# Optimization experiments

Hardware: AMD Instinct MI355X
Metric: run time of the kernel (lower is better)

The kernel has to match this reference:

```python
import jax, jax.numpy as jnp
import numpy as np

N_NODES = 50000

def _gcn_layer(x, src, dst, W, b, n_nodes):
    # x: [N, F_in]; src/dst: [E+N] (self-loops already appended)
    h = x @ W  # [N, F_out]
    deg = jax.ops.segment_sum(jnp.ones_like(dst, dtype=h.dtype), dst, num_segments=n_nodes)
    dinv = jnp.where(deg > 0, jax.lax.rsqrt(deg), 0.0)  # deg^{-1/2}
    norm = dinv[src] * dinv[dst]  # [E+N]
    msg = h[src] * norm[:, None]  # gather + scale
    out = jax.ops.segment_sum(msg, dst, num_segments=n_nodes)  # scatter-add
    return out + b

def setup_inputs() -> dict:
    key = jax.random.key(0)
    k1, k2, k3, k4 = jax.random.split(key, 4)
    d = 128
    E = 800000
    x = jax.random.normal(k1, (N_NODES, d), dtype=jnp.float32)
    edge_index = jax.random.randint(k2, (2, E), 0, N_NODES, dtype=jnp.int64)
    W1 = jax.random.normal(k3, (d, d), dtype=jnp.float32) / np.sqrt(d)
    b1 = jnp.zeros((d,), dtype=jnp.float32)
    W2 = jax.random.normal(k4, (d, d), dtype=jnp.float32) / np.sqrt(d)
    b2 = jnp.zeros((d,), dtype=jnp.float32)
    return {"x": x, "edge_index": edge_index, "W1": W1, "b1": b1, "W2": W2, "b2": b2}

def reference(x, edge_index, W1, b1, W2, b2):
    n = x.shape[0]
    loops = jnp.arange(n, dtype=edge_index.dtype)
    src = jnp.concatenate([edge_index[0], loops])  # add self-loops
    dst = jnp.concatenate([edge_index[1], loops])
    h = _gcn_layer(x, src, dst, W1, b1, n)
    h = jax.nn.relu(h)
    z = _gcn_layer(h, src, dst, W2, b2, n)
    return z
```

## Files before the change

kernel.cpp:

```cpp
#include <hip/hip_runtime.h>
#include <hip/hip_fp16.h>

#define NF 128
#define KC 64
#define NPART 4
#define NPMAX 12544

typedef _Float16 half8  __attribute__((ext_vector_type(8)));
typedef _Float16 half4v __attribute__((ext_vector_type(4)));
typedef float    floatx4 __attribute__((ext_vector_type(4)));

__global__ __launch_bounds__(512) void count2_k(
    const int* __restrict__ dst, unsigned char* __restrict__ pcnt,
    int E, int N, int Ec)
{
    __shared__ int lcnt[NPMAX];
    const int p = blockIdx.x & 3, c = blockIdx.x >> 2;
    const int Np = (N + 3) >> 2;
    const int lo = p * Np, hi = min(lo + Np, N);
    const int sz = hi - lo;
    for (int i = threadIdx.x; i < sz; i += 512) lcnt[i] = 0;
    __syncthreads();

    const int e0 = c * Ec, e1 = min(e0 + Ec, E);
    for (int e = e0 + (int)threadIdx.x * 4; e + 3 < e1; e += 512 * 4) {
        int4 d = *(const int4*)(dst + e);
        if (d.x >= lo && d.x < hi) atomicAdd(&lcnt[d.x - lo], 1);
        if (d.y >= lo && d.y < hi) atomicAdd(&lcnt[d.y - lo], 1);
        if (d.z >= lo && d.z < hi) atomicAdd(&lcnt[d.z - lo], 1);
        if (d.w >= lo && d.w < hi) atomicAdd(&lcnt[d.w - lo], 1);
    }
    int rem0 = e0 + ((e1 - e0) & ~3);
    for (int e = rem0 + (int)threadIdx.x; e < e1; e += 512) {
        int d = dst[e];
        if (d >= lo && d < hi) atomicAdd(&lcnt[d - lo], 1);
    }
    __syncthreads();
    for (int i = threadIdx.x; i < sz; i += 512)
        pcnt[(size_t)c * N + lo + i] = (unsigned char)lcnt[i];
}

__global__ __launch_bounds__(256) void pscan2_k(
    unsigned char* __restrict__ pcnt, float* __restrict__ dinv,
    int* __restrict__ rowptr, int* __restrict__ blocksum, int n, int N, int nb,
    const float* __restrict__ W1, const float* __restrict__ W2,
    __half* __restrict__ WT1, __half* __restrict__ WT2)
{
    if ((int)blockIdx.x >= nb) {
        int idx = ((int)blockIdx.x - nb) * 256 + threadIdx.x;
        const float* W = (idx < 16384) ? W1 : W2;
        __half* WT     = (idx < 16384) ? WT1 : WT2;
        int j = idx & 16383;
        int nn = j & 127, k = j >> 7;
        WT[nn * NF + k] = __float2half(W[k * NF + nn]);
        return;
    }
    __shared__ int sm[256];
    int tid = threadIdx.x;
    int bin = blockIdx.x * 256 + tid;
    int total = 0;
    if (bin < n) {
        #pragma unroll 4
        for (int c = 0; c < KC; c++) {
            size_t o = (size_t)c * N + bin;
            int v = pcnt[o];
            pcnt[o] = (unsigned char)total;
            total += v;
        }
        dinv[bin] = rsqrtf((float)total + 1.0f);
    }
    sm[tid] = total;
    __syncthreads();
    #pragma unroll
    for (int d = 1; d < 256; d <<= 1) {
        int t = (tid >= d) ? sm[tid - d] : 0;
        __syncthreads();
        sm[tid] += t;
        __syncthreads();
    }
    if (bin < n) rowptr[bin] = sm[tid] - total;
    if (tid == 255) blocksum[blockIdx.x] = sm[255];
}

template<bool F32IN>
__device__ __forceinline__ void gemm_body512(
    const void* __restrict__ Xv, const __half* __restrict__ WT,
    const float* __restrict__ dinv, __half* __restrict__ out, int M, int bid,
    __half (*wlds)[136])
{
    const int tid = threadIdx.x;
    {
        int r = tid >> 2;
        int c0 = (tid & 3) * 32;
        const half8* s = (const half8*)(WT + (size_t)r * NF + c0);
        half8* d = (half8*)&wlds[r][c0];
        #pragma unroll
        for (int j = 0; j < 4; j++) d[j] = s[j];
    }
    __syncthreads();

    const int wave = tid >> 6, lane = tid & 63;
    const int quad = lane >> 4, l15 = lane & 15;
    const int rowA = bid * 128 + wave * 16 + l15;
    const int rowc = (rowA < M) ? rowA : (M - 1);

    half8 afr[4];
    if (F32IN) {
        const float* X = (const float*)Xv;
        #pragma unroll
        for (int kc = 0; kc < 4; kc++) {
            const floatx4* p = (const floatx4*)(X + (size_t)rowc * NF + kc * 32 + quad * 8);
            floatx4 u = p[0], v = p[1];
            half8 a;
            a[0] = (_Float16)u[0]; a[1] = (_Float16)u[1];
            a[2] = (_Float16)u[2]; a[3] = (_Float16)u[3];
            a[4] = (_Float16)v[0]; a[5] = (_Float16)v[1];
            a[6] = (_Float16)v[2]; a[7] = (_Float16)v[3];
            afr[kc] = a;
        }
    } else {
        const __half* X = (const __half*)Xv;
        #pragma unroll
        for (int kc = 0; kc < 4; kc++)
            afr[kc] = *(const half8*)(X + (size_t)rowc * NF + kc * 32 + quad * 8);
    }

    floatx4 acc[8];
    #pragma unroll
    for (int ct = 0; ct < 8; ct++) { floatx4 z = {0.f, 0.f, 0.f, 0.f}; acc[ct] = z; }

    #pragma unroll
    for (int kc = 0; kc < 4; kc++) {
        #pragma unroll
        for (int ct = 0; ct < 8; ct++) {
            half8 b = *(const half8*)&wlds[ct * 16 + l15][kc * 32 + quad * 8];
            acc[ct] = __builtin_amdgcn_mfma_f32_16x16x32_f16(afr[kc], b, acc[ct], 0, 0, 0);
        }
    }

    const int orow0 = bid * 128 + wave * 16 + quad * 4;
    #pragma unroll
    for (int r = 0; r < 4; r++) {
        int orow = orow0 + r;
        if (orow < M) {
            float s = dinv[orow];
            #pragma unroll
            for (int ct = 0; ct < 8; ct++)
                out[(size_t)orow * NF + ct * 16 + l15] = __float2half(acc[ct][r] * s);
        }
    }
}

__global__ __launch_bounds__(512) void mid_k(
    const int* __restrict__ src, const int* __restrict__ dst,
    const int* __restrict__ rowptr, const unsigned char* __restrict__ coff,
    const int* __restrict__ blocksum, int* __restrict__ rowptr2,
    int* __restrict__ csr, int E, int N, int Ec, int nb,
    const float* __restrict__ X, const __half* __restrict__ WT,
    const float* __restrict__ dinv, __half* __restrict__ H, int GB2)
{
    __shared__ __align__(16) char smem[NPMAX * 4 + 1024];
    const int tid = threadIdx.x;
    if ((int)blockIdx.x < GB2) {
        gemm_body512<true>(X, WT, dinv, H, N, blockIdx.x, (__half(*)[136])smem);
        return;
    }
    int* lcur = (int*)smem;
    int* pref = (int*)(smem + NPMAX * 4);

    const int b = blockIdx.x - GB2;
    const int p = b & 3, c = b >> 2;
    const int Np = (N + 3) >> 2;
    const int lo = p * Np, hi = min(lo + Np, N);
    const int sz = hi - lo;

    int v = (tid < nb) ? blocksum[tid] : 0;
    if (tid < 256) pref[tid] = v;
    __syncthreads();
    #pragma unroll
    for (int d = 1; d < 256; d <<= 1) {
        int t = (tid < 256 && tid >= d) ? pref[tid - d] : 0;
        __syncthreads();
        if (tid < 256) pref[tid] += t;
        __syncthreads();
    }
    if (tid < 256) pref[tid] -= v;
    __syncthreads();

    for (int i = tid; i < sz; i += 512) {
        int bin = lo + i;
        int r = rowptr[bin] + pref[bin >> 8] + (int)coff[(size_t)c * N + bin];
        lcur[i] = r;
        if (c == 0) rowptr2[bin] = r;
    }
    if (c == 0 && p == 0 && tid == 0) rowptr2[N] = E;
    __syncthreads();

    const int e0 = c * Ec, e1 = min(e0 + Ec, E);
    for (int e = e0 + tid * 4; e + 3 < e1; e += 512 * 4) {
        int4 d = *(const int4*)(dst + e);
        int4 s = *(const int4*)(src + e);
        if (d.x >= lo && d.x < hi) csr[atomicAdd(&lcur[d.x - lo], 1)] = s.x;
        if (d.y >= lo && d.y < hi) csr[atomicAdd(&lcur[d.y - lo], 1)] = s.y;
        if (d.z >= lo && d.z < hi) csr[atomicAdd(&lcur[d.z - lo], 1)] = s.z;
        if (d.w >= lo && d.w < hi) csr[atomicAdd(&lcur[d.w - lo], 1)] = s.w;
    }
    int rem0 = e0 + ((e1 - e0) & ~3);
    for (int e = rem0 + tid; e < e1; e += 512) {
        int d = dst[e];
        if (d >= lo && d < hi) csr[atomicAdd(&lcur[d - lo], 1)] = src[e];
    }
}

__device__ __forceinline__ floatx4 gather_acc(
    const half4v* __restrict__ hs4, const int* __restrict__ csr,
    int base, int cnt, int node, int eg, int fl, int lane)
{
    floatx4 acc = {0.f, 0.f, 0.f, 0.f};
    int m0 = min(64, cnt);
    int idx0 = 0;
    if (lane < m0) idx0 = __builtin_nontemporal_load(&csr[base + lane]);
    if (eg == 0) {
        half4v s = hs4[(size_t)node * 32 + fl];
        acc[0] = (float)s[0]; acc[1] = (float)s[1];
        acc[2] = (float)s[2]; acc[3] = (float)s[3];
    }
    for (int off = 0; off < cnt; off += 64) {
        int m = min(64, cnt - off);
        int idx = (off == 0) ? idx0 : 0;
        if (off && lane < m) idx = __builtin_nontemporal_load(&csr[base + off + lane]);
        for (int j = 0; j < m; j += 16) {
            int s[8];
            half4v v[8];
            #pragma unroll
            for (int t = 0; t < 8; t++)
                s[t] = __shfl(idx, min(j + 2 * t + eg, m - 1), 64);
            #pragma unroll
            for (int t = 0; t < 8; t++)
                v[t] = hs4[(size_t)s[t] * 32 + fl];
            #pragma unroll
            for (int t = 0; t < 8; t++) {
                if (j + 2 * t + eg < m) {
                    acc[0] += (float)v[t][0]; acc[1] += (float)v[t][1];
                    acc[2] += (float)v[t][2]; acc[3] += (float)v[t][3];
                }
            }
        }
    }
    #pragma unroll
    for (int k = 0; k < 4; k++) acc[k] += __shfl_xor(acc[k], 32, 64);
    return acc;
}

__global__ __launch_bounds__(256) void agg_k(
    const __half* __restrict__ hs, const int* __restrict__ rowptr,
    const int* __restrict__ csr, const float* __restrict__ dinv,
    const float* __restrict__ bias, __half* __restrict__ outh,
    float* __restrict__ outf, int n)
{
    int wave = threadIdx.x >> 6;
    int lane = threadIdx.x & 63;
    int node = blockIdx.x * 4 + wave;
    if (node >= n) return;
    const int eg = lane >> 5, fl = lane & 31;

    int base = rowptr[node];
    int cnt  = rowptr[node + 1] - base;
    floatx4 acc = gather_acc((const half4v*)hs, csr, base, cnt, node, eg, fl, lane);

    if (eg == 0) {
        float dv = dinv[node];
        float o0 = dv * acc[0] + bias[fl * 4 + 0];
        float o1 = dv * acc[1] + bias[fl * 4 + 1];
        float o2 = dv * acc[2] + bias[fl * 4 + 2];
        float o3 = dv * acc[3] + bias[fl * 4 + 3];
        if (outh) {
            half4v h;
            h[0] = (_Float16)fmaxf(o0, 0.f); h[1] = (_Float16)fmaxf(o1, 0.f);
            h[2] = (_Float16)fmaxf(o2, 0.f); h[3] = (_Float16)fmaxf(o3, 0.f);
            *(half4v*)&outh[(size_t)node * NF + fl * 4] = h;
        } else {
            floatx4 w = {o0, o1, o2, o3};
            *(floatx4*)(outf + (size_t)node * NF + fl * 4) = w;
        }
    }
}

__global__ __launch_bounds__(256) void aggmm_k(
    const __half* __restrict__ hs, const int* __restrict__ rowptr,
    const int* __restrict__ csr, const float* __restrict__ dinv,
    const float* __restrict__ bias, const __half* __restrict__ WT,
    __half* __restrict__ Hout, int n)
{
    __shared__ __half alds[16][136];
    const int tid = threadIdx.x;
    const int wave = tid >> 6, lane = tid & 63;
    const int eg = lane >> 5, fl = lane & 31;
    const int nb0 = blockIdx.x * 16;

    #pragma unroll 1
    for (int q = 0; q < 4; q++) {
        int node = nb0 + wave * 4 + q;
        if (node < n) {
            int base = rowptr[node];
            int cnt  = rowptr[node + 1] - base;
            floatx4 acc = gather_acc((const half4v*)hs, csr, base, cnt, node, eg, fl, lane);
            if (eg == 0) {
                float dv = dinv[node];
                half4v h;
                h[0] = (_Float16)fmaxf(dv * acc[0] + bias[fl * 4 + 0], 0.f);
                h[1] = (_Float16)fmaxf(dv * acc[1] + bias[fl * 4 + 1], 0.f);
                h[2] = (_Float16)fmaxf(dv * acc[2] + bias[fl * 4 + 2], 0.f);
                h[3] = (_Float16)fmaxf(dv * acc[3] + bias[fl * 4 + 3], 0.f);
                *(half4v*)&alds[wave * 4 + q][fl * 4] = h;
            }
        } else if (eg == 0) {
            half4v z = {(_Float16)0.f, (_Float16)0.f, (_Float16)0.f, (_Float16)0.f};
            *(half4v*)&alds[wave * 4 + q][fl * 4] = z;
        }
    }
    __syncthreads();

    const int quad = lane >> 4, l15 = lane & 15;
    half8 afr[4];
    #pragma unroll
    for (int kc = 0; kc < 4; kc++)
        afr[kc] = *(const half8*)&alds[l15][kc * 32 + quad * 8];

    floatx4 acc0 = {0.f, 0.f, 0.f, 0.f};
    floatx4 acc1 = {0.f, 0.f, 0.f, 0.f};
    const int ct0 = wave * 2, ct1 = wave * 2 + 1;
    #pragma unroll
    for (int kc = 0; kc < 4; kc++) {
        half8 b0 = *(const half8*)(WT + (size_t)(ct0 * 16 + l15) * NF + kc * 32 + quad * 8);
        half8 b1 = *(const half8*)(WT + (size_t)(ct1 * 16 + l15) * NF + kc * 32 + quad * 8);
        acc0 = __builtin_amdgcn_mfma_f32_16x16x32_f16(afr[kc], b0, acc0, 0, 0, 0);
        acc1 = __builtin_amdgcn_mfma_f32_16x16x32_f16(afr[kc], b1, acc1, 0, 0, 0);
    }

    #pragma unroll
    for (int r = 0; r < 4; r++) {
        int row = quad * 4 + r;
        int node = nb0 + row;
        if (node < n) {
            float s = dinv[node];
            Hout[(size_t)node * NF + ct0 * 16 + l15] = __float2half(acc0[r] * s);
            Hout[(size_t)node * NF + ct1 * 16 + l15] = __float2half(acc1[r] * s);
        }
    }
}


extern "C" void kernel_launch(void* const* d_in, const int* in_sizes, int n_in,
                              void* d_out, int out_size, void* d_ws, size_t ws_size,
                              hipStream_t stream) {
    const float* x  = (const float*)d_in[0];
    const int*   ei = (const int*)d_in[1];
    const float* W1 = (const float*)d_in[2];
    const float* b1 = (const float*)d_in[3];
    const float* W2 = (const float*)d_in[4];
    const float* b2 = (const float*)d_in[5];
    float* out = (float*)d_out;

    const int N = in_sizes[0] / NF;
    const int E = in_sizes[1] / 2;
    const int* src = ei;
    const int* dst = ei + E;

    char* ws = (char*)d_ws;
    size_t off = 0;
    auto alloc = [&](size_t bytes) {
        void* p = ws + off;
        off += bytes;
        off = (off + 63) & ~(size_t)63;
        return p;
    };
    unsigned char* pcnt = (unsigned char*)alloc((size_t)KC * N);
    int*    rowptr  = (int*)alloc((size_t)(N + 1) * 4);
    int*    rowptr2 = (int*)alloc((size_t)(N + 1) * 4);
    int*    csr     = (int*)alloc((size_t)E * 4);
    float*  dinv    = (float*)alloc((size_t)N * 4);
    int*    bsum    = (int*)alloc((size_t)256 * 4);
    __half* WT1     = (__half*)alloc((size_t)NF * NF * 2);
    __half* WT2     = (__half*)alloc((size_t)NF * NF * 2);
    __half* H16     = (__half*)alloc((size_t)N * NF * 2);
    __half* A16     = (__half*)alloc((size_t)N * NF * 2);

    int nb  = (N + 255) / 256;
    int Ec  = (((E + KC - 1) / KC) + 3) & ~3;
    int GB2 = (N + 127) / 128;
    int fb  = (N + 15) / 16;
    int ab  = (N + 3) / 4;

    count2_k<<<KC * NPART, 512, 0, stream>>>(dst, pcnt, E, N, Ec);
    pscan2_k<<<nb + 128, 256, 0, stream>>>(pcnt, dinv, rowptr, bsum, N, N, nb,
                                           W1, W2, WT1, WT2);
    mid_k<<<GB2 + KC * NPART, 512, 0, stream>>>(src, dst, rowptr, pcnt, bsum,
                                                rowptr2, csr, E, N, Ec, nb,
                                                x, WT1, dinv, H16, GB2);
    aggmm_k<<<fb, 256, 0, stream>>>(H16, rowptr2, csr, dinv, b1, WT2, A16, N);
    agg_k<<<ab, 256, 0, stream>>>(A16, rowptr2, csr, dinv, b2, nullptr, out, N);
}
```

Measured before the change: 206.9 us.

## Sort CSR neighbor lists and interleave gathers across four nodes per wave

Adds a bitonic sort kernel that orders each node's source indices inside 64-entry chunks, so gathered rows come in ascending address order and may get better cache locality. The gather routine is replaced by one that processes four nodes per wave at once, interleaving their neighbor loads to raise memory-level parallelism. The final aggregation kernel now handles 16 nodes per block this way. This costs an extra kernel launch and a sort pass over the whole CSR. Small-degree nodes also lose the 8-wide unrolled batch of loads.

```diff
diff --git a/kernel.cpp b/kernel.cpp
--- a/kernel.cpp
+++ b/kernel.cpp
@@ -212,77 +212,103 @@
     }
 }
 
-__device__ __forceinline__ floatx4 gather_acc(
-    const half4v* __restrict__ hs4, const int* __restrict__ csr,
-    int base, int cnt, int node, int eg, int fl, int lane)
-{
-    floatx4 acc = {0.f, 0.f, 0.f, 0.f};
-    int m0 = min(64, cnt);
-    int idx0 = 0;
-    if (lane < m0) idx0 = __builtin_nontemporal_load(&csr[base + lane]);
-    if (eg == 0) {
-        half4v s = hs4[(size_t)node * 32 + fl];
-        acc[0] = (float)s[0]; acc[1] = (float)s[1];
-        acc[2] = (float)s[2]; acc[3] = (float)s[3];
-    }
+__global__ __launch_bounds__(256) void bsort_k(
+    const int* __restrict__ rowptr, int* __restrict__ csr, int n)
+{
+    int wave = threadIdx.x >> 6, lane = threadIdx.x & 63;
+    int node = blockIdx.x * 4 + wave;
+    if (node >= n) return;
+    int base = rowptr[node], cnt = rowptr[node + 1] - base;
     for (int off = 0; off < cnt; off += 64) {
         int m = min(64, cnt - off);
-        int idx = (off == 0) ? idx0 : 0;
-        if (off && lane < m) idx = __builtin_nontemporal_load(&csr[base + off + lane]);
-        for (int j = 0; j < m; j += 16) {
-            int s[8];
-            half4v v[8];
+        if (m <= 1) break;
+        int v = (lane < m) ? csr[base + off + lane] : 0x7fffffff;
+        #pragma unroll
+        for (int k = 2; k <= 64; k <<= 1) {
             #pragma unroll
-            for (int t = 0; t < 8; t++)
-                s[t] = __shfl(idx, min(j + 2 * t + eg, m - 1), 64);
-            #pragma unroll
-            for (int t = 0; t < 8; t++)
-                v[t] = hs4[(size_t)s[t] * 32 + fl];
-            #pragma unroll
-            for (int t = 0; t < 8; t++) {
-                if (j + 2 * t + eg < m) {
-                    acc[0] += (float)v[t][0]; acc[1] += (float)v[t][1];
-                    acc[2] += (float)v[t][2]; acc[3] += (float)v[t][3];
+            for (int j = k >> 1; j >= 1; j >>= 1) {
+                int pv = __shfl_xor(v, j, 64);
+                bool up = ((lane & k) == 0);
+                bool mn = (((lane & j) == 0) == up);
+                v = mn ? min(v, pv) : max(v, pv);
+            }
+        }
+        if (lane < m) csr[base + off + lane] = v;
+    }
+}
+
+__device__ __forceinline__ void gather4s(
+    const half4v* __restrict__ hs4, const int* __restrict__ csr,
+    const int* __restrict__ rowptr, int node0, int n,
+    int eg, int fl, int lane, floatx4 acc[4])
+{
+    int base[4], cc[4], rc[4], idx[4];
+    int maxc = 0;
+    #pragma unroll
+    for (int k = 0; k < 4; k++) {
+        int nd = node0 + k;
+        int b0 = 0, c0 = 0;
+        if (nd < n) { b0 = rowptr[nd]; c0 = rowptr[nd + 1] - b0; }
+        base[k] = b0; rc[k] = c0; cc[k] = min(c0, 64);
+        maxc = max(maxc, cc[k]);
+    }
+    #pragma unroll
+    for (int k = 0; k < 4; k++)
+        idx[k] = (lane < cc[k]) ? __builtin_nontemporal_load(&csr[base[k] + lane]) : 0;
+
+    #pragma unroll
+    for (int k = 0; k < 4; k++) { floatx4 z = {0.f, 0.f, 0.f, 0.f}; acc[k] = z; }
+
+    if (eg == 0) {
+        #pragma unroll
+        for (int k = 0; k < 4; k++) {
+            int nd = node0 + k;
+            if (nd < n) {
+                half4v s = hs4[(size_t)nd * 32 + fl];
+                acc[k][0] += (float)s[0]; acc[k][1] += (float)s[1];
+                acc[k][2] += (float)s[2]; acc[k][3] += (float)s[3];
+            }
+        }
+    }
+
+    const int rmax = (maxc + 1) >> 1;
+    #pragma unroll 2
+    for (int s = 0; s < rmax; s++) {
+        const int e2 = s * 2;
+        #pragma unroll
+        for (int k = 0; k < 4; k++) {
+            if (e2 < cc[k]) {
+                int si = __shfl(idx[k], min(e2 + eg, cc[k] - 1), 64);
+                half4v v = hs4[(size_t)si * 32 + fl];
+                if (e2 + eg < cc[k]) {
+                    acc[k][0] += (float)v[0]; acc[k][1] += (float)v[1];
+                    acc[k][2] += (float)v[2]; acc[k][3] += (float)v[3];
                 }
             }
         }
     }
-    #pragma unroll
-    for (int k = 0; k < 4; k++) acc[k] += __shfl_xor(acc[k], 32, 64);
-    return acc;
-}
-
-__global__ __launch_bounds__(256) void agg_k(
-    const __half* __restrict__ hs, const int* __restrict__ rowptr,
-    const int* __restrict__ csr, const float* __restrict__ dinv,
-    const float* __restrict__ bias, __half* __restrict__ outh,
-    float* __restrict__ outf, int n)
-{
-    int wave = threadIdx.x >> 6;
-    int lane = threadIdx.x & 63;
-    int node = blockIdx.x * 4 + wave;
-    if (node >= n) return;
-    const int eg = lane >> 5, fl = lane & 31;
-
-    int base = rowptr[node];
-    int cnt  = rowptr[node + 1] - base;
-    floatx4 acc = gather_acc((const half4v*)hs, csr, base, cnt, node, eg, fl, lane);
-
-    if (eg == 0) {
-        float dv = dinv[node];
-        float o0 = dv * acc[0] + bias[fl * 4 + 0];
-        float o1 = dv * acc[1] + bias[fl * 4 + 1];
-        float o2 = dv * acc[2] + bias[fl * 4 + 2];
-        float o3 = dv * acc[3] + bias[fl * 4 + 3];
-        if (outh) {
-            half4v h;
-            h[0] = (_Float16)fmaxf(o0, 0.f); h[1] = (_Float16)fmaxf(o1, 0.f);
-            h[2] = (_Float16)fmaxf(o2, 0.f); h[3] = (_Float16)fmaxf(o3, 0.f);
-            *(half4v*)&outh[(size_t)node * NF + fl * 4] = h;
-        } else {
-            floatx4 w = {o0, o1, o2, o3};
-            *(floatx4*)(outf + (size_t)node * NF + fl * 4) = w;
-        }
+
+    #pragma unroll
+    for (int k = 0; k < 4; k++) {
+        for (int off = 64; off < rc[k]; off += 64) {
+            int m = min(64, rc[k] - off);
+            int id2 = (lane < m) ? __builtin_nontemporal_load(&csr[base[k] + off + lane]) : 0;
+            for (int j = 0; j < m; j += 2) {
+                int si = __shfl(id2, min(j + eg, m - 1), 64);
+                half4v v = hs4[(size_t)si * 32 + fl];
+                if (j + eg < m) {
+                    acc[k][0] += (float)v[0]; acc[k][1] += (float)v[1];
+                    acc[k][2] += (float)v[2]; acc[k][3] += (float)v[3];
+                }
+            }
+        }
+    }
+
+    #pragma unroll
+    for (int k = 0; k < 4; k++) {
+        #pragma unroll
+        for (int q = 0; q < 4; q++)
+            acc[k][q] += __shfl_xor(acc[k][q], 32, 64);
     }
 }
 
@@ -297,26 +323,27 @@
     const int wave = tid >> 6, lane = tid & 63;
     const int eg = lane >> 5, fl = lane & 31;
     const int nb0 = blockIdx.x * 16;
-
-    #pragma unroll 1
-    for (int q = 0; q < 4; q++) {
-        int node = nb0 + wave * 4 + q;
-        if (node < n) {
-            int base = rowptr[node];
-            int cnt  = rowptr[node + 1] - base;
-            floatx4 acc = gather_acc((const half4v*)hs, csr, base, cnt, node, eg, fl, lane);
-            if (eg == 0) {
+    const int node0 = nb0 + wave * 4;
+
+    floatx4 acc[4];
+    gather4s((const half4v*)hs, csr, rowptr, node0, n, eg, fl, lane, acc);
+
+    if (eg == 0) {
+        #pragma unroll
+        for (int k = 0; k < 4; k++) {
+            int node = node0 + k;
+            half4v h;
+            if (node < n) {
                 float dv = dinv[node];
-                half4v h;
-                h[0] = (_Float16)fmaxf(dv * acc[0] + bias[fl * 4 + 0], 0.f);
-                h[1] = (_Float16)fmaxf(dv * acc[1] + bias[fl * 4 + 1], 0.f);
-                h[2] = (_Float16)fmaxf(dv * acc[2] + bias[fl * 4 + 2], 0.f);
-                h[3] = (_Float16)fmaxf(dv * acc[3] + bias[fl * 4 + 3], 0.f);
-                *(half4v*)&alds[wave * 4 + q][fl * 4] = h;
-            }
-        } else if (eg == 0) {
-            half4v z = {(_Float16)0.f, (_Float16)0.f, (_Float16)0.f, (_Float16)0.f};
-            *(half4v*)&alds[wave * 4 + q][fl * 4] = z;
+                h[0] = (_Float16)fmaxf(dv * acc[k][0] + bias[fl * 4 + 0], 0.f);
+                h[1] = (_Float16)fmaxf(dv * acc[k][1] + bias[fl * 4 + 1], 0.f);
+                h[2] = (_Float16)fmaxf(dv * acc[k][2] + bias[fl * 4 + 2], 0.f);
+                h[3] = (_Float16)fmaxf(dv * acc[k][3] + bias[fl * 4 + 3], 0.f);
+            } else {
+                h[0] = (_Float16)0.f; h[1] = (_Float16)0.f;
+                h[2] = (_Float16)0.f; h[3] = (_Float16)0.f;
+            }
+            *(half4v*)&alds[wave * 4 + k][fl * 4] = h;
         }
     }
     __syncthreads();
@@ -346,6 +373,36 @@
             float s = dinv[node];
             Hout[(size_t)node * NF + ct0 * 16 + l15] = __float2half(acc0[r] * s);
             Hout[(size_t)node * NF + ct1 * 16 + l15] = __float2half(acc1[r] * s);
+        }
+    }
+}
+
+__global__ __launch_bounds__(256) void agg4_k(
+    const __half* __restrict__ hs, const int* __restrict__ rowptr,
+    const int* __restrict__ csr, const float* __restrict__ dinv,
+    const float* __restrict__ bias, float* __restrict__ outf, int n)
+{
+    const int tid = threadIdx.x;
+    const int wave = tid >> 6, lane = tid & 63;
+    const int eg = lane >> 5, fl = lane & 31;
+    const int node0 = blockIdx.x * 16 + wave * 4;
+
+    floatx4 acc[4];
+    gather4s((const half4v*)hs, csr, rowptr, node0, n, eg, fl, lane, acc);
+
+    if (eg == 0) {
+        #pragma unroll
+        for (int k = 0; k < 4; k++) {
+            int node = node0 + k;
+            if (node < n) {
+                float dv = dinv[node];
+                floatx4 w;
+                w[0] = dv * acc[k][0] + bias[fl * 4 + 0];
+                w[1] = dv * acc[k][1] + bias[fl * 4 + 1];
+                w[2] = dv * acc[k][2] + bias[fl * 4 + 2];
+                w[3] = dv * acc[k][3] + bias[fl * 4 + 3];
+                *(floatx4*)(outf + (size_t)node * NF + fl * 4) = w;
+            }
         }
     }
 }
@@ -389,8 +446,8 @@
     int nb  = (N + 255) / 256;
     int Ec  = (((E + KC - 1) / KC) + 3) & ~3;
     int GB2 = (N + 127) / 128;
+    int sb  = (N + 3) / 4;
     int fb  = (N + 15) / 16;
-    int ab  = (N + 3) / 4;
 
     count2_k<<<KC * NPART, 512, 0, stream>>>(dst, pcnt, E, N, Ec);
     pscan2_k<<<nb + 128, 256, 0, stream>>>(pcnt, dinv, rowptr, bsum, N, N, nb,
@@ -398,6 +455,7 @@
     mid_k<<<GB2 + KC * NPART, 512, 0, stream>>>(src, dst, rowptr, pcnt, bsum,
                                                 rowptr2, csr, E, N, Ec, nb,
                                                 x, WT1, dinv, H16, GB2);
+    bsort_k<<<sb, 256, 0, stream>>>(rowptr2, csr, N);
     aggmm_k<<<fb, 256, 0, stream>>>(H16, rowptr2, csr, dinv, b1, WT2, A16, N);
-    agg_k<<<ab, 256, 0, stream>>>(A16, rowptr2, csr, dinv, b2, nullptr, out, N);
-}
+    agg4_k<<<fb, 256, 0, stream>>>(A16, rowptr2, csr, dinv, b2, out, N);
+}
```

Result: slower. 233.3 us (+12.8%).

## Gather eight nodes per wave with double-buffered interleaved loads in aggregation kernels

Applied to the files above, without the earlier changes.

Both aggregation kernels now give each wave eight destination nodes and keep two sets of eight gather loads in flight, alternating between them, so memory latency is hidden across nodes rather than within one node's short edge list. The aggmm kernel grows to 32 nodes per block with four MFMA tiles per wave, and the final layer uses a matching agg4 kernel. Nodes with more than 64 neighbours fall back to a serial tail loop. The cost is much higher register pressure, which is mitigated with a launch bound of four blocks per CU, and lanes idle when degrees within a group of eight differ.

```diff
diff --git a/kernel.cpp b/kernel.cpp
--- a/kernel.cpp
+++ b/kernel.cpp
@@ -212,141 +212,212 @@
     }
 }
 
-__device__ __forceinline__ floatx4 gather_acc(
-    const half4v* __restrict__ hs4, const int* __restrict__ csr,
-    int base, int cnt, int node, int eg, int fl, int lane)
-{
-    floatx4 acc = {0.f, 0.f, 0.f, 0.f};
-    int m0 = min(64, cnt);
-    int idx0 = 0;
-    if (lane < m0) idx0 = __builtin_nontemporal_load(&csr[base + lane]);
-    if (eg == 0) {
-        half4v s = hs4[(size_t)node * 32 + fl];
-        acc[0] = (float)s[0]; acc[1] = (float)s[1];
-        acc[2] = (float)s[2]; acc[3] = (float)s[3];
-    }
-    for (int off = 0; off < cnt; off += 64) {
-        int m = min(64, cnt - off);
-        int idx = (off == 0) ? idx0 : 0;
-        if (off && lane < m) idx = __builtin_nontemporal_load(&csr[base + off + lane]);
-        for (int j = 0; j < m; j += 16) {
-            int s[8];
-            half4v v[8];
-            #pragma unroll
-            for (int t = 0; t < 8; t++)
-                s[t] = __shfl(idx, min(j + 2 * t + eg, m - 1), 64);
-            #pragma unroll
-            for (int t = 0; t < 8; t++)
-                v[t] = hs4[(size_t)s[t] * 32 + fl];
-            #pragma unroll
-            for (int t = 0; t < 8; t++) {
-                if (j + 2 * t + eg < m) {
-                    acc[0] += (float)v[t][0]; acc[1] += (float)v[t][1];
-                    acc[2] += (float)v[t][2]; acc[3] += (float)v[t][3];
-                }
-            }
-        }
-    }
-    #pragma unroll
-    for (int k = 0; k < 4; k++) acc[k] += __shfl_xor(acc[k], 32, 64);
-    return acc;
-}
-
-__global__ __launch_bounds__(256) void agg_k(
-    const __half* __restrict__ hs, const int* __restrict__ rowptr,
-    const int* __restrict__ csr, const float* __restrict__ dinv,
-    const float* __restrict__ bias, __half* __restrict__ outh,
-    float* __restrict__ outf, int n)
-{
-    int wave = threadIdx.x >> 6;
-    int lane = threadIdx.x & 63;
-    int node = blockIdx.x * 4 + wave;
-    if (node >= n) return;
-    const int eg = lane >> 5, fl = lane & 31;
-
-    int base = rowptr[node];
-    int cnt  = rowptr[node + 1] - base;
-    floatx4 acc = gather_acc((const half4v*)hs, csr, base, cnt, node, eg, fl, lane);
-
-    if (eg == 0) {
-        float dv = dinv[node];
-        float o0 = dv * acc[0] + bias[fl * 4 + 0];
-        float o1 = dv * acc[1] + bias[fl * 4 + 1];
-        float o2 = dv * acc[2] + bias[fl * 4 + 2];
-        float o3 = dv * acc[3] + bias[fl * 4 + 3];
-        if (outh) {
-            half4v h;
-            h[0] = (_Float16)fmaxf(o0, 0.f); h[1] = (_Float16)fmaxf(o1, 0.f);
-            h[2] = (_Float16)fmaxf(o2, 0.f); h[3] = (_Float16)fmaxf(o3, 0.f);
-            *(half4v*)&outh[(size_t)node * NF + fl * 4] = h;
-        } else {
-            floatx4 w = {o0, o1, o2, o3};
-            *(floatx4*)(outf + (size_t)node * NF + fl * 4) = w;
-        }
-    }
-}
-
-__global__ __launch_bounds__(256) void aggmm_k(
+#define G8_SETUP(K)                                                          \
+    int cc##K; int ix##K;                                                    \
+    {                                                                        \
+        int bs = 0, rcv = 0;                                                 \
+        if (node0 + K < n) { bs = rowptr[node0 + K];                         \
+                             rcv = rowptr[node0 + K + 1] - bs; }             \
+        cc##K = min(rcv, 64);                                                \
+        anytail |= (rcv > 64);                                               \
+        maxc = max(maxc, cc##K);                                             \
+        ix##K = (lane < cc##K)                                               \
+              ? __builtin_nontemporal_load(&csr[bs + lane]) : 0;             \
+    }
+
+#define G8_ISS1(X, K, s2)                                                    \
+    { int t = min((s2) + eg, cc##K - 1); t = (t < 0) ? 0 : t;                \
+      v##X##K = hs4[(size_t)__shfl(ix##K, t, 64) * 32 + fl]; }
+
+#define G8_ISSUE(X, s)                                                       \
+    { const int s2_ = (s) * 2;                                               \
+      G8_ISS1(X, 0, s2_) G8_ISS1(X, 1, s2_) G8_ISS1(X, 2, s2_)               \
+      G8_ISS1(X, 3, s2_) G8_ISS1(X, 4, s2_) G8_ISS1(X, 5, s2_)               \
+      G8_ISS1(X, 6, s2_) G8_ISS1(X, 7, s2_) }
+
+#define G8_AC1(X, K, s2)                                                     \
+    if ((s2) + eg < cc##K) {                                                 \
+        a##K[0] += (float)v##X##K[0]; a##K[1] += (float)v##X##K[1];          \
+        a##K[2] += (float)v##X##K[2]; a##K[3] += (float)v##X##K[3]; }
+
+#define G8_ACC(X, s)                                                         \
+    { const int s2_ = (s) * 2;                                               \
+      G8_AC1(X, 0, s2_) G8_AC1(X, 1, s2_) G8_AC1(X, 2, s2_)                  \
+      G8_AC1(X, 3, s2_) G8_AC1(X, 4, s2_) G8_AC1(X, 5, s2_)                  \
+      G8_AC1(X, 6, s2_) G8_AC1(X, 7, s2_) }
+
+#define G8_SELF(K)                                                           \
+    { int nd = min(node0 + K, n - 1);                                        \
+      half4v sl = hs4[(size_t)nd * 32 + fl];                                 \
+      if (node0 + K < n) {                                                   \
+          a##K[0] += (float)sl[0]; a##K[1] += (float)sl[1];                  \
+          a##K[2] += (float)sl[2]; a##K[3] += (float)sl[3]; } }
+
+#define G8_TAIL(K)                                                           \
+    {                                                                        \
+        int bs = rowptr[node0 + K];                                          \
+        int rcv = rowptr[node0 + K + 1] - bs;                                \
+        for (int off = 64; off < rcv; off += 64) {                           \
+            int m = min(64, rcv - off);                                      \
+            int id2 = (lane < m) ? csr[bs + off + lane] : 0;                 \
+            for (int j = 0; j < m; j += 2) {                                 \
+                int si = __shfl(id2, min(j + eg, m - 1), 64);                \
+                half4v vv = hs4[(size_t)si * 32 + fl];                       \
+                if (j + eg < m) {                                            \
+                    a##K[0] += (float)vv[0]; a##K[1] += (float)vv[1];        \
+                    a##K[2] += (float)vv[2]; a##K[3] += (float)vv[3]; }      \
+            }                                                                \
+        }                                                                    \
+    }
+
+#define G8_RED(K)                                                            \
+    { a##K[0] += __shfl_xor(a##K[0], 32, 64);                                \
+      a##K[1] += __shfl_xor(a##K[1], 32, 64);                                \
+      a##K[2] += __shfl_xor(a##K[2], 32, 64);                                \
+      a##K[3] += __shfl_xor(a##K[3], 32, 64); }
+
+#define GATHER8_BODY(hs4, csr, rowptr, node0, n, eg, fl, lane)               \
+    floatx4 a0 = {0,0,0,0}, a1 = {0,0,0,0}, a2 = {0,0,0,0}, a3 = {0,0,0,0};  \
+    floatx4 a4 = {0,0,0,0}, a5 = {0,0,0,0}, a6 = {0,0,0,0}, a7 = {0,0,0,0};  \
+    {                                                                        \
+        int maxc = 0; bool anytail = false;                                  \
+        G8_SETUP(0) G8_SETUP(1) G8_SETUP(2) G8_SETUP(3)                      \
+        G8_SETUP(4) G8_SETUP(5) G8_SETUP(6) G8_SETUP(7)                      \
+        if (eg == 0) {                                                       \
+            G8_SELF(0) G8_SELF(1) G8_SELF(2) G8_SELF(3)                      \
+            G8_SELF(4) G8_SELF(5) G8_SELF(6) G8_SELF(7)                      \
+        }                                                                    \
+        half4v vA0, vA1, vA2, vA3, vA4, vA5, vA6, vA7;                       \
+        half4v vB0, vB1, vB2, vB3, vB4, vB5, vB6, vB7;                       \
+        const int rmax = (maxc + 1) >> 1;                                    \
+        G8_ISSUE(A, 0)                                                       \
+        G8_ISSUE(B, 1)                                                       \
+        int s = 0;                                                           \
+        for (; s + 2 < rmax; s += 2) {                                       \
+            G8_ACC(A, s)     G8_ISSUE(A, s + 2)                              \
+            G8_ACC(B, s + 1) G8_ISSUE(B, s + 3)                              \
+        }                                                                    \
+        if (s < rmax)     { G8_ACC(A, s) }                                   \
+        if (s + 1 < rmax) { G8_ACC(B, s + 1) }                               \
+        if (anytail) {                                                       \
+            G8_TAIL(0) G8_TAIL(1) G8_TAIL(2) G8_TAIL(3)                      \
+            G8_TAIL(4) G8_TAIL(5) G8_TAIL(6) G8_TAIL(7)                      \
+        }                                                                    \
+        G8_RED(0) G8_RED(1) G8_RED(2) G8_RED(3)                              \
+        G8_RED(4) G8_RED(5) G8_RED(6) G8_RED(7)                              \
+    }
+
+__global__ __launch_bounds__(256, 4) void aggmm_k(
     const __half* __restrict__ hs, const int* __restrict__ rowptr,
     const int* __restrict__ csr, const float* __restrict__ dinv,
     const float* __restrict__ bias, const __half* __restrict__ WT,
     __half* __restrict__ Hout, int n)
 {
-    __shared__ __half alds[16][136];
+    __shared__ __half alds[32][136];
     const int tid = threadIdx.x;
     const int wave = tid >> 6, lane = tid & 63;
     const int eg = lane >> 5, fl = lane & 31;
-    const int nb0 = blockIdx.x * 16;
-
-    #pragma unroll 1
-    for (int q = 0; q < 4; q++) {
-        int node = nb0 + wave * 4 + q;
-        if (node < n) {
-            int base = rowptr[node];
-            int cnt  = rowptr[node + 1] - base;
-            floatx4 acc = gather_acc((const half4v*)hs, csr, base, cnt, node, eg, fl, lane);
-            if (eg == 0) {
-                float dv = dinv[node];
-                half4v h;
-                h[0] = (_Float16)fmaxf(dv * acc[0] + bias[fl * 4 + 0], 0.f);
-                h[1] = (_Float16)fmaxf(dv * acc[1] + bias[fl * 4 + 1], 0.f);
-                h[2] = (_Float16)fmaxf(dv * acc[2] + bias[fl * 4 + 2], 0.f);
-                h[3] = (_Float16)fmaxf(dv * acc[3] + bias[fl * 4 + 3], 0.f);
-                *(half4v*)&alds[wave * 4 + q][fl * 4] = h;
-            }
-        } else if (eg == 0) {
-            half4v z = {(_Float16)0.f, (_Float16)0.f, (_Float16)0.f, (_Float16)0.f};
-            *(half4v*)&alds[wave * 4 + q][fl * 4] = z;
-        }
+    const int nb0 = blockIdx.x * 32;
+    const int node0 = nb0 + wave * 8;
+    const half4v* hs4 = (const half4v*)hs;
+
+    GATHER8_BODY(hs4, csr, rowptr, node0, n, eg, fl, lane)
+
+    if (eg == 0) {
+        const float bv0 = bias[fl * 4 + 0], bv1 = bias[fl * 4 + 1];
+        const float bv2 = bias[fl * 4 + 2], bv3 = bias[fl * 4 + 3];
+        #define STORE_ALDS(K)                                                 \
+        {                                                                     \
+            int node = node0 + K;                                             \
+            half4v h;                                                         \
+            if (node < n) {                                                   \
+                float dv = dinv[node];                                        \
+                h[0] = (_Float16)fmaxf(dv * a##K[0] + bv0, 0.f);              \
+                h[1] = (_Float16)fmaxf(dv * a##K[1] + bv1, 0.f);              \
+                h[2] = (_Float16)fmaxf(dv * a##K[2] + bv2, 0.f);              \
+                h[3] = (_Float16)fmaxf(dv * a##K[3] + bv3, 0.f);              \
+            } else {                                                          \
+                h[0] = (_Float16)0.f; h[1] = (_Float16)0.f;                   \
+                h[2] = (_Float16)0.f; h[3] = (_Float16)0.f;                   \
+            }                                                                 \
+            *(half4v*)&alds[wave * 8 + K][fl * 4] = h;                        \
+        }
+        STORE_ALDS(0) STORE_ALDS(1) STORE_ALDS(2) STORE_ALDS(3)
+        STORE_ALDS(4) STORE_ALDS(5) STORE_ALDS(6) STORE_ALDS(7)
+        #undef STORE_ALDS
     }
     __syncthreads();
 
     const int quad = lane >> 4, l15 = lane & 15;
-    half8 afr[4];
-    #pragma unroll
-    for (int kc = 0; kc < 4; kc++)
-        afr[kc] = *(const half8*)&alds[l15][kc * 32 + quad * 8];
-
-    floatx4 acc0 = {0.f, 0.f, 0.f, 0.f};
-    floatx4 acc1 = {0.f, 0.f, 0.f, 0.f};
+    half8 afr0[4], afr1[4];
+    #pragma unroll
+    for (int kc = 0; kc < 4; kc++) {
+        afr0[kc] = *(const half8*)&alds[l15][kc * 32 + quad * 8];
+        afr1[kc] = *(const half8*)&alds[16 + l15][kc * 32 + quad * 8];
+    }
+
+    floatx4 o00 = {0.f, 0.f, 0.f, 0.f}, o01 = {0.f, 0.f, 0.f, 0.f};
+    floatx4 o10 = {0.f, 0.f, 0.f, 0.f}, o11 = {0.f, 0.f, 0.f, 0.f};
     const int ct0 = wave * 2, ct1 = wave * 2 + 1;
     #pragma unroll
     for (int kc = 0; kc < 4; kc++) {
         half8 b0 = *(const half8*)(WT + (size_t)(ct0 * 16 + l15) * NF + kc * 32 + quad * 8);
         half8 b1 = *(const half8*)(WT + (size_t)(ct1 * 16 + l15) * NF + kc * 32 + quad * 8);
-        acc0 = __builtin_amdgcn_mfma_f32_16x16x32_f16(afr[kc], b0, acc0, 0, 0, 0);
-        acc1 = __builtin_amdgcn_mfma_f32_16x16x32_f16(afr[kc], b1, acc1, 0, 0, 0);
+        o00 = __builtin_amdgcn_mfma_f32_16x16x32_f16(afr0[kc], b0, o00, 0, 0, 0);
+        o01 = __builtin_amdgcn_mfma_f32_16x16x32_f16(afr0[kc], b1, o01, 0, 0, 0);
+        o10 = __builtin_amdgcn_mfma_f32_16x16x32_f16(afr1[kc], b0, o10, 0, 0, 0);
+        o11 = __builtin_amdgcn_mfma_f32_16x16x32_f16(afr1[kc], b1, o11, 0, 0, 0);
     }
 
     #pragma unroll
     for (int r = 0; r < 4; r++) {
-        int row = quad * 4 + r;
-        int node = nb0 + row;
-        if (node < n) {
-            float s = dinv[node];
-            Hout[(size_t)node * NF + ct0 * 16 + l15] = __float2half(acc0[r] * s);
-            Hout[(size_t)node * NF + ct1 * 16 + l15] = __float2half(acc1[r] * s);
-        }
+        int n0 = nb0 + quad * 4 + r;
+        int n1 = n0 + 16;
+        if (n0 < n) {
+            float s = dinv[n0];
+            Hout[(size_t)n0 * NF + ct0 * 16 + l15] = __float2half(o00[r] * s);
+            Hout[(size_t)n0 * NF + ct1 * 16 + l15] = __float2half(o01[r] * s);
+        }
+        if (n1 < n) {
+            float s = dinv[n1];
+            Hout[(size_t)n1 * NF + ct0 * 16 + l15] = __float2half(o10[r] * s);
+            Hout[(size_t)n1 * NF + ct1 * 16 + l15] = __float2half(o11[r] * s);
+        }
+    }
+}
+
+__global__ __launch_bounds__(256, 4) void agg4_k(
+    const __half* __restrict__ hs, const int* __restrict__ rowptr,
+    const int* __restrict__ csr, const float* __restrict__ dinv,
+    const float* __restrict__ bias, float* __restrict__ outf, int n)
+{
+    const int tid = threadIdx.x;
+    const int wave = tid >> 6, lane = tid & 63;
+    const int eg = lane >> 5, fl = lane & 31;
+    const int node0 = blockIdx.x * 32 + wave * 8;
+    const half4v* hs4 = (const half4v*)hs;
+
+    GATHER8_BODY(hs4, csr, rowptr, node0, n, eg, fl, lane)
+
+    if (eg == 0) {
+        const float bv0 = bias[fl * 4 + 0], bv1 = bias[fl * 4 + 1];
+        const float bv2 = bias[fl * 4 + 2], bv3 = bias[fl * 4 + 3];
+        #define STORE_OUT(K)                                                  \
+        {                                                                     \
+            int node = node0 + K;                                             \
+            if (node < n) {                                                   \
+                float dv = dinv[node];                                        \
+                floatx4 w;                                                    \
+                w[0] = dv * a##K[0] + bv0;                                    \
+                w[1] = dv * a##K[1] + bv1;                                    \
+                w[2] = dv * a##K[2] + bv2;                                    \
+                w[3] = dv * a##K[3] + bv3;                                    \
+                *(floatx4*)(outf + (size_t)node * NF + fl * 4) = w;           \
+            }                                                                 \
+        }
+        STORE_OUT(0) STORE_OUT(1) STORE_OUT(2) STORE_OUT(3)
+        STORE_OUT(4) STORE_OUT(5) STORE_OUT(6) STORE_OUT(7)
+        #undef STORE_OUT
     }
 }
 
@@ -389,8 +460,7 @@
     int nb  = (N + 255) / 256;
     int Ec  = (((E + KC - 1) / KC) + 3) & ~3;
     int GB2 = (N + 127) / 128;
-    int fb  = (N + 15) / 16;
-    int ab  = (N + 3) / 4;
+    int fb  = (N + 31) / 32;
 
     count2_k<<<KC * NPART, 512, 0, stream>>>(dst, pcnt, E, N, Ec);
     pscan2_k<<<nb + 128, 256, 0, stream>>>(pcnt, dinv, rowptr, bsum, N, N, nb,
@@ -399,5 +469,5 @@
                                                 rowptr2, csr, E, N, Ec, nb,
                                                 x, WT1, dinv, H16, GB2);
     aggmm_k<<<fb, 256, 0, stream>>>(H16, rowptr2, csr, dinv, b1, WT2, A16, N);
-    agg_k<<<ab, 256, 0, stream>>>(A16, rowptr2, csr, dinv, b2, nullptr, out, N);
-}
+    agg4_k<<<fb, 256, 0, stream>>>(A16, rowptr2, csr, dinv, b2, out, N);
+}
```

Measured after the change: 468.1 us. 126% more time.

## Gather two nodes per wave with 16-byte row loads and wider aggregation blocks

Applied to the files above, without the earlier changes.

Replaces the one-node-per-wave gather with a routine where each wave handles two adjacent nodes, using four 16-lane groups and half8 (16-byte) feature loads. Each lane covers 8 features and every edge split is reduced with a shuffle across 16 lanes. The fused aggregate+matmul kernel grows to 512 threads, so each wave gathers two nodes and computes one output column tile instead of two. The aim is more memory-level parallelism and wider loads for the irregular gathers. The cost is extra shuffles and wasted lanes when the two nodes have different degrees.

```diff
diff --git a/kernel.cpp b/kernel.cpp
--- a/kernel.cpp
+++ b/kernel.cpp
@@ -212,81 +212,109 @@
     }
 }
 
-__device__ __forceinline__ floatx4 gather_acc(
-    const half4v* __restrict__ hs4, const int* __restrict__ csr,
-    int base, int cnt, int node, int eg, int fl, int lane)
-{
-    floatx4 acc = {0.f, 0.f, 0.f, 0.f};
-    int m0 = min(64, cnt);
-    int idx0 = 0;
-    if (lane < m0) idx0 = __builtin_nontemporal_load(&csr[base + lane]);
-    if (eg == 0) {
-        half4v s = hs4[(size_t)node * 32 + fl];
-        acc[0] = (float)s[0]; acc[1] = (float)s[1];
-        acc[2] = (float)s[2]; acc[3] = (float)s[3];
-    }
-    for (int off = 0; off < cnt; off += 64) {
-        int m = min(64, cnt - off);
-        int idx = (off == 0) ? idx0 : 0;
-        if (off && lane < m) idx = __builtin_nontemporal_load(&csr[base + off + lane]);
-        for (int j = 0; j < m; j += 16) {
+__device__ __forceinline__ void gather2w(
+    const half8* __restrict__ hs8, const int* __restrict__ csr,
+    const int* __restrict__ rowptr, int nA, int n,
+    int g, int fl, int lane, floatx4& ac0, floatx4& ac1)
+{
+    const int ep  = g & 1;
+    const int isB = g >> 1;
+    const int nB  = nA + 1;
+
+    int baseA = 0, cntA = 0, baseB = 0, cntB = 0;
+    if (nA < n) {
+        baseA = rowptr[nA];
+        int mid = rowptr[nA + 1];
+        cntA = mid - baseA;
+        if (nB < n) { baseB = mid; cntB = rowptr[nB + 1] - mid; }
+    }
+    const int ccA = min(cntA, 64), ccB = min(cntB, 64);
+
+    int idxA = (lane < ccA) ? __builtin_nontemporal_load(&csr[baseA + lane]) : 0;
+    int idxB = (lane < ccB) ? __builtin_nontemporal_load(&csr[baseB + lane]) : 0;
+
+    if (ep == 0) {
+        int nd = isB ? nB : nA;
+        if (nd < n) {
+            half8 s = hs8[(size_t)nd * 16 + fl];
+            ac0[0] += (float)s[0]; ac0[1] += (float)s[1];
+            ac0[2] += (float)s[2]; ac0[3] += (float)s[3];
+            ac1[0] += (float)s[4]; ac1[1] += (float)s[5];
+            ac1[2] += (float)s[6]; ac1[3] += (float)s[7];
+        }
+    }
+
+    const int myc  = isB ? ccB : ccA;
+    const int maxc = max(ccA, ccB);
+    for (int j = 0; j < maxc; j += 16) {
+        int s[8];
+        half8 v[8];
+        #pragma unroll
+        for (int t = 0; t < 8; t++) {
+            int e = j + 2 * t + ep;
+            int eA = min(e, ccA - 1); eA = (eA < 0) ? 0 : eA;
+            int eB = min(e, ccB - 1); eB = (eB < 0) ? 0 : eB;
+            int sa = __shfl(idxA, eA, 64);
+            int sb = __shfl(idxB, eB, 64);
+            s[t] = isB ? sb : sa;
+        }
+        #pragma unroll
+        for (int t = 0; t < 8; t++)
+            v[t] = hs8[(size_t)s[t] * 16 + fl];
+        #pragma unroll
+        for (int t = 0; t < 8; t++) {
+            if (j + 2 * t + ep < myc) {
+                ac0[0] += (float)v[t][0]; ac0[1] += (float)v[t][1];
+                ac0[2] += (float)v[t][2]; ac0[3] += (float)v[t][3];
+                ac1[0] += (float)v[t][4]; ac1[1] += (float)v[t][5];
+                ac1[2] += (float)v[t][6]; ac1[3] += (float)v[t][7];
+            }
+        }
+    }
+
+    const int cmax = max(cntA, cntB);
+    for (int off = 64; off < cmax; off += 64) {
+        int cA2 = cntA - off; cA2 = (cA2 < 0) ? 0 : min(cA2, 64);
+        int cB2 = cntB - off; cB2 = (cB2 < 0) ? 0 : min(cB2, 64);
+        int iA2 = (lane < cA2) ? csr[baseA + off + lane] : 0;
+        int iB2 = (lane < cB2) ? csr[baseB + off + lane] : 0;
+        int myc2 = isB ? cB2 : cA2;
+        int m2   = max(cA2, cB2);
+        for (int j = 0; j < m2; j += 16) {
             int s[8];
-            half4v v[8];
+            half8 v[8];
+            #pragma unroll
+            for (int t = 0; t < 8; t++) {
+                int e = j + 2 * t + ep;
+                int eA = min(e, cA2 - 1); eA = (eA < 0) ? 0 : eA;
+                int eB = min(e, cB2 - 1); eB = (eB < 0) ? 0 : eB;
+                int sa = __shfl(iA2, eA, 64);
+                int sb = __shfl(iB2, eB, 64);
+                s[t] = isB ? sb : sa;
+            }
             #pragma unroll
             for (int t = 0; t < 8; t++)
-                s[t] = __shfl(idx, min(j + 2 * t + eg, m - 1), 64);
-            #pragma unroll
-            for (int t = 0; t < 8; t++)
-                v[t] = hs4[(size_t)s[t] * 32 + fl];
+                v[t] = hs8[(size_t)s[t] * 16 + fl];
             #pragma unroll
             for (int t = 0; t < 8; t++) {
-                if (j + 2 * t + eg < m) {
-                    acc[0] += (float)v[t][0]; acc[1] += (float)v[t][1];
-                    acc[2] += (float)v[t][2]; acc[3] += (float)v[t][3];
+                if (j + 2 * t + ep < myc2) {
+                    ac0[0] += (float)v[t][0]; ac0[1] += (float)v[t][1];
+                    ac0[2] += (float)v[t][2]; ac0[3] += (float)v[t][3];
+                    ac1[0] += (float)v[t][4]; ac1[1] += (float)v[t][5];
+                    ac1[2] += (float)v[t][6]; ac1[3] += (float)v[t][7];
                 }
             }
         }
     }
-    #pragma unroll
-    for (int k = 0; k < 4; k++) acc[k] += __shfl_xor(acc[k], 32, 64);
-    return acc;
-}
-
-__global__ __launch_bounds__(256) void agg_k(
-    const __half* __restrict__ hs, const int* __restrict__ rowptr,
-    const int* __restrict__ csr, const float* __restrict__ dinv,
-    const float* __restrict__ bias, __half* __restrict__ outh,
-    float* __restrict__ outf, int n)
-{
-    int wave = threadIdx.x >> 6;
-    int lane = threadIdx.x & 63;
-    int node = blockIdx.x * 4 + wave;
-    if (node >= n) return;
-    const int eg = lane >> 5, fl = lane & 31;
-
-    int base = rowptr[node];
-    int cnt  = rowptr[node + 1] - base;
-    floatx4 acc = gather_acc((const half4v*)hs, csr, base, cnt, node, eg, fl, lane);
-
-    if (eg == 0) {
-        float dv = dinv[node];
-        float o0 = dv * acc[0] + bias[fl * 4 + 0];
-        float o1 = dv * acc[1] + bias[fl * 4 + 1];
-        float o2 = dv * acc[2] + bias[fl * 4 + 2];
-        float o3 = dv * acc[3] + bias[fl * 4 + 3];
-        if (outh) {
-            half4v h;
-            h[0] = (_Float16)fmaxf(o0, 0.f); h[1] = (_Float16)fmaxf(o1, 0.f);
-            h[2] = (_Float16)fmaxf(o2, 0.f); h[3] = (_Float16)fmaxf(o3, 0.f);
-            *(half4v*)&outh[(size_t)node * NF + fl * 4] = h;
-        } else {
-            floatx4 w = {o0, o1, o2, o3};
-            *(floatx4*)(outf + (size_t)node * NF + fl * 4) = w;
-        }
-    }
-}
-
-__global__ __launch_bounds__(256) void aggmm_k(
+
+    #pragma unroll
+    for (int q = 0; q < 4; q++) {
+        ac0[q] += __shfl_xor(ac0[q], 16, 64);
+        ac1[q] += __shfl_xor(ac1[q], 16, 64);
+    }
+}
+
+__global__ __launch_bounds__(512) void aggmm_k(
     const __half* __restrict__ hs, const int* __restrict__ rowptr,
     const int* __restrict__ csr, const float* __restrict__ dinv,
     const float* __restrict__ bias, const __half* __restrict__ WT,
@@ -295,57 +323,88 @@
     __shared__ __half alds[16][136];
     const int tid = threadIdx.x;
     const int wave = tid >> 6, lane = tid & 63;
-    const int eg = lane >> 5, fl = lane & 31;
+    const int g = lane >> 4, fl = lane & 15;
     const int nb0 = blockIdx.x * 16;
-
-    #pragma unroll 1
-    for (int q = 0; q < 4; q++) {
-        int node = nb0 + wave * 4 + q;
+    const int nA = nb0 + wave * 2;
+
+    floatx4 ac0 = {0.f, 0.f, 0.f, 0.f}, ac1 = {0.f, 0.f, 0.f, 0.f};
+    gather2w((const half8*)hs, csr, rowptr, nA, n, g, fl, lane, ac0, ac1);
+
+    if ((g & 1) == 0) {
+        int node = nA + (g >> 1);
+        int row  = wave * 2 + (g >> 1);
+        half8 hv;
         if (node < n) {
-            int base = rowptr[node];
-            int cnt  = rowptr[node + 1] - base;
-            floatx4 acc = gather_acc((const half4v*)hs, csr, base, cnt, node, eg, fl, lane);
-            if (eg == 0) {
-                float dv = dinv[node];
-                half4v h;
-                h[0] = (_Float16)fmaxf(dv * acc[0] + bias[fl * 4 + 0], 0.f);
-                h[1] = (_Float16)fmaxf(dv * acc[1] + bias[fl * 4 + 1], 0.f);
-                h[2] = (_Float16)fmaxf(dv * acc[2] + bias[fl * 4 + 2], 0.f);
-                h[3] = (_Float16)fmaxf(dv * acc[3] + bias[fl * 4 + 3], 0.f);
-                *(half4v*)&alds[wave * 4 + q][fl * 4] = h;
-            }
-        } else if (eg == 0) {
-            half4v z = {(_Float16)0.f, (_Float16)0.f, (_Float16)0.f, (_Float16)0.f};
-            *(half4v*)&alds[wave * 4 + q][fl * 4] = z;
-        }
+            float dv = dinv[node];
+            const floatx4 bv0 = *(const floatx4*)&bias[fl * 8];
+            const floatx4 bv1 = *(const floatx4*)&bias[fl * 8 + 4];
+            hv[0] = (_Float16)fmaxf(dv * ac0[0] + bv0[0], 0.f);
+            hv[1] = (_Float16)fmaxf(dv * ac0[1] + bv0[1], 0.f);
+            hv[2] = (_Float16)fmaxf(dv * ac0[2] + bv0[2], 0.f);
+            hv[3] = (_Float16)fmaxf(dv * ac0[3] + bv0[3], 0.f);
+            hv[4] = (_Float16)fmaxf(dv * ac1[0] + bv1[0], 0.f);
+            hv[5] = (_Float16)fmaxf(dv * ac1[1] + bv1[1], 0.f);
+            hv[6] = (_Float16)fmaxf(dv * ac1[2] + bv1[2], 0.f);
+            hv[7] = (_Float16)fmaxf(dv * ac1[3] + bv1[3], 0.f);
+        } else {
+            #pragma unroll
+            for (int i = 0; i < 8; i++) hv[i] = (_Float16)0.f;
+        }
+        *(half8*)&alds[row][fl * 8] = hv;
     }
     __syncthreads();
 
     const int quad = lane >> 4, l15 = lane & 15;
+    const int ct = wave;
     half8 afr[4];
     #pragma unroll
     for (int kc = 0; kc < 4; kc++)
         afr[kc] = *(const half8*)&alds[l15][kc * 32 + quad * 8];
 
-    floatx4 acc0 = {0.f, 0.f, 0.f, 0.f};
-    floatx4 acc1 = {0.f, 0.f, 0.f, 0.f};
-    const int ct0 = wave * 2, ct1 = wave * 2 + 1;
+    floatx4 o0 = {0.f, 0.f, 0.f, 0.f};
     #pragma unroll
     for (int kc = 0; kc < 4; kc++) {
-        half8 b0 = *(const half8*)(WT + (size_t)(ct0 * 16 + l15) * NF + kc * 32 + quad * 8);
-        half8 b1 = *(const half8*)(WT + (size_t)(ct1 * 16 + l15) * NF + kc * 32 + quad * 8);
-        acc0 = __builtin_amdgcn_mfma_f32_16x16x32_f16(afr[kc], b0, acc0, 0, 0, 0);
-        acc1 = __builtin_amdgcn_mfma_f32_16x16x32_f16(afr[kc], b1, acc1, 0, 0, 0);
+        half8 b = *(const half8*)(WT + (size_t)(ct * 16 + l15) * NF + kc * 32 + quad * 8);
+        o0 = __builtin_amdgcn_mfma_f32_16x16x32_f16(afr[kc], b, o0, 0, 0, 0);
     }
 
     #pragma unroll
     for (int r = 0; r < 4; r++) {
-        int row = quad * 4 + r;
-        int node = nb0 + row;
+        int node = nb0 + quad * 4 + r;
         if (node < n) {
             float s = dinv[node];
-            Hout[(size_t)node * NF + ct0 * 16 + l15] = __float2half(acc0[r] * s);
-            Hout[(size_t)node * NF + ct1 * 16 + l15] = __float2half(acc1[r] * s);
+            Hout[(size_t)node * NF + ct * 16 + l15] = __float2half(o0[r] * s);
+        }
+    }
+}
+
+__global__ __launch_bounds__(256) void agg4_k(
+    const __half* __restrict__ hs, const int* __restrict__ rowptr,
+    const int* __restrict__ csr, const float* __restrict__ dinv,
+    const float* __restrict__ bias, float* __restrict__ outf, int n)
+{
+    const int tid = threadIdx.x;
+    const int wave = tid >> 6, lane = tid & 63;
+    const int g = lane >> 4, fl = lane & 15;
+    const int nA = blockIdx.x * 8 + wave * 2;
+    if (nA >= n) return;
+
+    floatx4 ac0 = {0.f, 0.f, 0.f, 0.f}, ac1 = {0.f, 0.f, 0.f, 0.f};
+    gather2w((const half8*)hs, csr, rowptr, nA, n, g, fl, lane, ac0, ac1);
+
+    if ((g & 1) == 0) {
+        int node = nA + (g >> 1);
+        if (node < n) {
+            float dv = dinv[node];
+            const floatx4 bv0 = *(const floatx4*)&bias[fl * 8];
+            const floatx4 bv1 = *(const floatx4*)&bias[fl * 8 + 4];
+            floatx4 w0, w1;
+            w0[0] = dv * ac0[0] + bv0[0]; w0[1] = dv * ac0[1] + bv0[1];
+            w0[2] = dv * ac0[2] + bv0[2]; w0[3] = dv * ac0[3] + bv0[3];
+            w1[0] = dv * ac1[0] + bv1[0]; w1[1] = dv * ac1[1] + bv1[1];
+            w1[2] = dv * ac1[2] + bv1[2]; w1[3] = dv * ac1[3] + bv1[3];
+            *(floatx4*)(outf + (size_t)node * NF + fl * 8)     = w0;
+            *(floatx4*)(outf + (size_t)node * NF + fl * 8 + 4) = w1;
         }
     }
 }
@@ -390,7 +449,7 @@
     int Ec  = (((E + KC - 1) / KC) + 3) & ~3;
     int GB2 = (N + 127) / 128;
     int fb  = (N + 15) / 16;
-    int ab  = (N + 3) / 4;
+    int ab  = (N + 7) / 8;
 
     count2_k<<<KC * NPART, 512, 0, stream>>>(dst, pcnt, E, N, Ec);
     pscan2_k<<<nb + 128, 256, 0, stream>>>(pcnt, dinv, rowptr, bsum, N, N, nb,
@@ -398,6 +457,6 @@
     mid_k<<<GB2 + KC * NPART, 512, 0, stream>>>(src, dst, rowptr, pcnt, bsum,
                                                 rowptr2, csr, E, N, Ec, nb,
                                                 x, WT1, dinv, H16, GB2);
-    aggmm_k<<<fb, 256, 0, stream>>>(H16, rowptr2, csr, dinv, b1, WT2, A16, N);
-    agg_k<<<ab, 256, 0, stream>>>(A16, rowptr2, csr, dinv, b2, nullptr, out, N);
-}
+    aggmm_k<<<fb, 512, 0, stream>>>(H16, rowptr2, csr, dinv, b1, WT2, A16, N);
+    agg4_k<<<ab, 256, 0, stream>>>(A16, rowptr2, csr, dinv, b2, out, N);
+}
```

Result: no change. 204.3 us (median of 2 runs) (-1.2%).
